# Kernel tuning notes

Hardware: AMD Instinct MI355X
Metric: run time of the kernel (lower is better)

Reference implementation:

```python
import jax, jax.numpy as jnp
import numpy as np

NUM_HEADS = 8
GROUPS = 32  # min(32, 512 // 4)
EPS = 1e-5


def group_norm(y, gamma, beta):
    B, C, L = y.shape
    yg = y.reshape(B, GROUPS, -1)  # [B, G, (C//G)*L]
    mu = yg.mean(-1, keepdims=True)
    var = yg.var(-1, keepdims=True)
    yn = ((yg - mu) * jax.lax.rsqrt(var + EPS)).reshape(B, C, L)
    return yn * gamma[:, None] + beta[:, None]


def setup_inputs() -> dict:
    key = jax.random.key(0)
    ks = jax.random.split(key, 5)
    B, C, L = 4, 512, 2048
    return {
        "x": jax.random.normal(ks[0], (B, C, L), dtype=jnp.float32),
        "Wqkv": jax.random.normal(ks[1], (3 * C, C), dtype=jnp.float32) * (C ** -0.5),
        "bqkv": jax.random.normal(ks[2], (3 * C,), dtype=jnp.float32) * 0.01,
        "Wproj": jax.random.normal(ks[3], (C, C), dtype=jnp.float32) * (C ** -0.5),
        "bproj": jax.random.normal(ks[4], (C,), dtype=jnp.float32) * 0.01,
        "gamma": jnp.ones((C,), dtype=jnp.float32),
        "beta": jnp.zeros((C,), dtype=jnp.float32),
    }


def reference(x, Wqkv, bqkv, Wproj, bproj, gamma, beta):
    B, C, L = x.shape
    H = NUM_HEADS
    D = C // H
    # 1x1 Conv1d == channel-mixing matmul
    qkv = jnp.einsum('oc,bcl->bol', Wqkv, x) + bqkv[:, None]  # [B, 3C, L]
    qkv = qkv.reshape(B, 3, H, D, L)
    q, k, v = qkv[:, 0], qkv[:, 1], qkv[:, 2]
    q = jnp.clip(q, -10.0, 10.0)
    k = jnp.clip(k, -10.0, 10.0)
    v = jnp.clip(v, -10.0, 10.0)
    scale = D ** -0.5
    attn = jnp.einsum('bhdi,bhdj->bhij', q, k) * scale  # [B, H, L, L]
    attn = jnp.clip(attn, -10.0, 10.0)
    attn = jax.nn.softmax(attn, axis=-1)
    # NaN fallback: replace whole attn with identity if any NaN (matches torch branch)
    has_nan = jnp.isnan(attn).any()
    attn = jnp.where(has_nan, jnp.eye(L, dtype=x.dtype), attn)
    out = jnp.einsum('bhij,bhdj->bhdi', attn, v)  # [B, H, D, L]
    out = out.reshape(B, C, L)
    out = jnp.einsum('oc,bcl->bol', Wproj, out) + bproj[:, None]
    return group_norm(out + x, gamma, beta)
```

## Files before the change

### kernel.cpp

```cpp
#include <hip/hip_runtime.h>
#include <cstddef>

#define B_ 4
#define C_ 512
#define L_ 2048

typedef __attribute__((ext_vector_type(8))) short  short8;
typedef __attribute__((ext_vector_type(4))) float  f32x4;
typedef __attribute__((ext_vector_type(4))) unsigned short us4;

#define AS1 __attribute__((address_space(1)))
#define AS3 __attribute__((address_space(3)))

__device__ __forceinline__ float clip10(float v){ return fminf(fmaxf(v,-10.0f),10.0f); }

__device__ __forceinline__ unsigned short f2bf(float f){
  union { float f; unsigned u; } v; v.f = f;
  unsigned r = v.u + 0x7fffu + ((v.u >> 16) & 1u);
  return (unsigned short)(r >> 16);
}
__device__ __forceinline__ unsigned pk(float lo, float hi){
  return (unsigned)f2bf(lo) | ((unsigned)f2bf(hi) << 16);
}
__device__ __forceinline__ void gl16(const void* g, void* l){
  __builtin_amdgcn_global_load_lds((const AS1 unsigned*)g, (AS3 unsigned*)l, 16, 0, 0);
}

__global__ __launch_bounds__(256) void prep_k(
    const float* __restrict__ x, const float* __restrict__ Wq,
    const float* __restrict__ Wp, unsigned short* __restrict__ xT,
    unsigned short* __restrict__ Wqb, unsigned short* __restrict__ Wpb)
{
  const int blk = blockIdx.x;
  const int t = threadIdx.x;
  if (blk < 4096){
    __shared__ float tile[32][33];
    const int b = blk>>10, rem = blk&1023;
    const int c0 = (rem>>6)*32, l0 = (rem&63)*32;
    const int cr = t>>3, lc = (t&7)*4;
    const float4 v = *(const float4*)(x + ((size_t)b*C_ + c0+cr)*L_ + l0 + lc);
    tile[cr][lc]=v.x; tile[cr][lc+1]=v.y; tile[cr][lc+2]=v.z; tile[cr][lc+3]=v.w;
    __syncthreads();
    const int lr = t>>3, cc = (t&7)*4;
    const us4 o = { f2bf(tile[cc][lr]), f2bf(tile[cc+1][lr]),
                    f2bf(tile[cc+2][lr]), f2bf(tile[cc+3][lr]) };
    *(us4*)(xT + ((size_t)b*L_ + l0+lr)*C_ + c0 + cc) = o;
  } else {
    const int i = (blk-4096)*256 + t;
    const int NQ = 1536*512/4;
    const float* src; unsigned short* dst; int j;
    if (i < NQ){ src = Wq; dst = Wqb; j = i; }
    else       { src = Wp; dst = Wpb; j = i - NQ; }
    const float4 v = *(const float4*)(src + (size_t)j*4);
    const us4 o = { f2bf(v.x), f2bf(v.y), f2bf(v.z), f2bf(v.w) };
    *(us4*)(dst + (size_t)j*4) = o;
  }
}

template<int MODE>
__global__ __launch_bounds__(256) void mfma_gemm(
    const unsigned short* __restrict__ Wb, const unsigned short* __restrict__ Bin,
    const float* __restrict__ bias,
    unsigned short* __restrict__ qT, unsigned short* __restrict__ kT,
    unsigned short* __restrict__ vN, float* __restrict__ yout)
{
  __shared__ unsigned short SA[128*64];
  __shared__ unsigned short SB[128*64];
  const int t = threadIdx.x;
  const int b = blockIdx.z;
  const int mb = blockIdx.y, n0 = blockIdx.x*128, m0 = mb*128;
  const int lane = t&63, w = t>>6, wm = w>>1, wn = w&1;
  const int n = lane&15, q4 = lane>>4;

  f32x4 acc[4][4];
#pragma unroll
  for (int i=0;i<4;i++)
#pragma unroll
    for (int j=0;j<4;j++) acc[i][j] = (f32x4){0.f,0.f,0.f,0.f};

  const unsigned short* Arow = Wb + (size_t)m0*512;
  const unsigned short* Brow = Bin + ((size_t)b*L_ + n0)*512;

  for (int kt=0; kt<8; kt++){
    const int k0 = kt*64;
    __syncthreads();
#pragma unroll
    for (int i=0;i<4;i++){
      const int ch = t + 256*i;
      const int row = ch>>3, lc = (ch&7) ^ (row&7);
      gl16(Arow + (size_t)row*512 + k0 + lc*8, &SA[ch*8]);
      gl16(Brow + (size_t)row*512 + k0 + lc*8, &SB[ch*8]);
    }
    __syncthreads();
#pragma unroll
    for (int kk=0;kk<2;kk++){
      short8 aF[4], bF[4];
      const int pc = ((kk*4+q4) ^ (n&7))*8;
#pragma unroll
      for (int mt=0;mt<4;mt++) aF[mt] = *(const short8*)&SA[(wm*64+mt*16+n)*64 + pc];
#pragma unroll
      for (int nt=0;nt<4;nt++) bF[nt] = *(const short8*)&SB[(wn*64+nt*16+n)*64 + pc];
#pragma unroll
      for (int mt=0;mt<4;mt++)
#pragma unroll
        for (int nt=0;nt<4;nt++)
          acc[mt][nt] = __builtin_amdgcn_mfma_f32_16x16x32_bf16(aF[mt], bF[nt], acc[mt][nt], 0,0,0);
    }
  }

#pragma unroll
  for (int mt=0;mt<4;mt++){
    const int obase = m0 + wm*64 + mt*16 + q4*4;
    const float b0=bias[obase], b1=bias[obase+1], b2=bias[obase+2], b3=bias[obase+3];
#pragma unroll
    for (int nt=0;nt<4;nt++){
      const int l = n0 + wn*64 + nt*16 + n;
      float r0=acc[mt][nt][0]+b0, r1=acc[mt][nt][1]+b1,
            r2=acc[mt][nt][2]+b2, r3=acc[mt][nt][3]+b3;
      if (MODE==0){
        r0=clip10(r0); r1=clip10(r1); r2=clip10(r2); r3=clip10(r3);
        const int typ = mb>>2;
        const int oin = obase - typ*512;
        if (typ < 2){
          unsigned short* dst = (typ==0) ? qT : kT;
          const us4 o = { f2bf(r0), f2bf(r1), f2bf(r2), f2bf(r3) };
          *(us4*)&dst[((size_t)b*L_ + l)*512 + oin] = o;
        } else {
          unsigned short* dst = vN + ((size_t)b*512 + oin)*L_ + l;
          dst[0]=f2bf(r0); dst[(size_t)L_]=f2bf(r1);
          dst[(size_t)2*L_]=f2bf(r2); dst[(size_t)3*L_]=f2bf(r3);
        }
      } else {
        float* dst = yout + ((size_t)b*512 + obase)*L_ + l;
        dst[0]=r0; dst[(size_t)L_]=r1; dst[(size_t)2*L_]=r2; dst[(size_t)3*L_]=r3;
      }
    }
  }
}

#define PP 72

__global__ __launch_bounds__(256) void attn_v4(
    const unsigned short* __restrict__ qT, const unsigned short* __restrict__ kT,
    const unsigned short* __restrict__ vN, unsigned short* __restrict__ attnT)
{
  __shared__ unsigned short s_p[128*PP];
  __shared__ unsigned short s_kv[2][2][64*64];
  const int t  = threadIdx.x;
  const int i0 = blockIdx.x*128;
  const int h  = blockIdx.y, b = blockIdx.z;
  const int lane = t&63, w = t>>6, n = lane&15, q4 = lane>>4;

  const unsigned short* kb0 = kT + (size_t)b*L_*512 + h*64;
  const unsigned short* vb  = vN + ((size_t)b*512 + h*64)*L_;

  short8 qf[2][2];
#pragma unroll
  for (int mt=0; mt<2; mt++)
#pragma unroll
    for (int kk=0; kk<2; kk++)
      qf[mt][kk] = *(const short8*)(qT + ((size_t)b*L_ + i0 + w*32 + mt*16 + n)*512
                                       + h*64 + kk*32 + q4*8);

#pragma unroll
  for (int i=0;i<2;i++){
    const int ch = t + 256*i, row = ch>>3, lc = (ch&7)^(row&7);
    gl16(kb0 + (size_t)row*512 + lc*8, &s_kv[0][0][ch*8]);
    gl16(vb  + (size_t)row*L_  + lc*8, &s_kv[0][1][ch*8]);
  }

  f32x4 oacc[2][4];
  float dacc[2];
#pragma unroll
  for (int mt=0;mt<2;mt++){ dacc[mt]=0.f;
#pragma unroll
    for (int dt=0;dt<4;dt++) oacc[mt][dt]=(f32x4){0.f,0.f,0.f,0.f}; }

  const float SCL = 0.125f*1.44269504089f;
  const float LIM = 14.4269504089f;

  int p = 0;
  for (int j0=0; j0<L_; j0+=64, p^=1){
    __syncthreads();
    if (j0+64 < L_){
#pragma unroll
      for (int i=0;i<2;i++){
        const int ch = t + 256*i, row = ch>>3, lc = (ch&7)^(row&7);
        gl16(kb0 + (size_t)(j0+64+row)*512 + lc*8,  &s_kv[p^1][0][ch*8]);
        gl16(vb  + (size_t)row*L_ + (j0+64) + lc*8, &s_kv[p^1][1][ch*8]);
      }
    }
    const unsigned short* sk = s_kv[p][0];
    const unsigned short* sv = s_kv[p][1];

    f32x4 sacc[2][4];
#pragma unroll
    for (int mt=0;mt<2;mt++)
#pragma unroll
      for (int jt=0;jt<4;jt++) sacc[mt][jt]=(f32x4){0.f,0.f,0.f,0.f};
#pragma unroll
    for (int kk=0;kk<2;kk++){
      const int pc = ((kk*4+q4) ^ (n&7))*8;
      short8 aK[4];
#pragma unroll
      for (int jt=0;jt<4;jt++) aK[jt] = *(const short8*)&sk[(jt*16+n)*64 + pc];
#pragma unroll
      for (int mt=0;mt<2;mt++)
#pragma unroll
        for (int jt=0;jt<4;jt++)
          sacc[mt][jt] = __builtin_amdgcn_mfma_f32_16x16x32_bf16(aK[jt], qf[mt][kk], sacc[mt][jt], 0,0,0);
    }

#pragma unroll
    for (int mt=0;mt<2;mt++)
#pragma unroll
      for (int jt=0;jt<4;jt++){
        const float e0 = __builtin_amdgcn_exp2f(__builtin_amdgcn_fmed3f(sacc[mt][jt][0]*SCL,-LIM,LIM));
        const float e1 = __builtin_amdgcn_exp2f(__builtin_amdgcn_fmed3f(sacc[mt][jt][1]*SCL,-LIM,LIM));
        const float e2 = __builtin_amdgcn_exp2f(__builtin_amdgcn_fmed3f(sacc[mt][jt][2]*SCL,-LIM,LIM));
        const float e3 = __builtin_amdgcn_exp2f(__builtin_amdgcn_fmed3f(sacc[mt][jt][3]*SCL,-LIM,LIM));
        dacc[mt] += (e0+e1)+(e2+e3);
        const unsigned long long pv =
            (unsigned long long)pk(e0,e1) | ((unsigned long long)pk(e2,e3)<<32);
        *(unsigned long long*)&s_p[(w*32 + mt*16 + n)*PP + jt*16 + q4*4] = pv;
      }

#pragma unroll
    for (int kk=0;kk<2;kk++){
      const int pcv = ((kk*4+q4) ^ (n&7))*8;
      short8 bV[4], pA[2];
#pragma unroll
      for (int dt=0;dt<4;dt++) bV[dt] = *(const short8*)&sv[(dt*16+n)*64 + pcv];
#pragma unroll
      for (int mt=0;mt<2;mt++)
        pA[mt] = *(const short8*)&s_p[(w*32 + mt*16 + n)*PP + kk*32 + q4*8];
#pragma unroll
      for (int mt=0;mt<2;mt++)
#pragma unroll
        for (int dt=0;dt<4;dt++)
          oacc[mt][dt] = __builtin_amdgcn_mfma_f32_16x16x32_bf16(pA[mt], bV[dt], oacc[mt][dt], 0,0,0);
    }
  }

  float inv[2];
#pragma unroll
  for (int mt=0;mt<2;mt++){
    float d = dacc[mt];
    d += __shfl_xor(d, 16);
    d += __shfl_xor(d, 32);
    inv[mt] = 1.0f/d;
  }
  float invr[2][4];
#pragma unroll
  for (int mt=0;mt<2;mt++)
#pragma unroll
    for (int r=0;r<4;r++)
      invr[mt][r] = __shfl(inv[mt], q4*4 + r);

#pragma unroll
  for (int mt=0;mt<2;mt++)
#pragma unroll
    for (int dt=0;dt<4;dt++)
#pragma unroll
      for (int r=0;r<4;r++){
        const size_t off = ((size_t)b*L_ + i0 + w*32 + mt*16 + q4*4 + r)*512 + h*64 + dt*16 + n;
        attnT[off] = f2bf(oacc[mt][dt][r]*invr[mt][r]);
      }
}

__global__ __launch_bounds__(256) void gn_stats(
    const float* __restrict__ y, const float* __restrict__ x,
    float* __restrict__ part)
{
  const int blk = blockIdx.x;
  const int b = blk>>7, g = (blk>>2)&31, s = blk&3;
  const size_t base = ((size_t)b*C_ + g*16)*L_ + s*512;
  const int t = threadIdx.x;
  float sum=0.f, sq=0.f;
#pragma unroll
  for (int i=0;i<8;i++){
    const int e = i*256 + t;
    const size_t off = base + (size_t)(e>>7)*L_ + (e&127)*4;
    const float4 vy=*(const float4*)(y+off);
    const float4 vx=*(const float4*)(x+off);
    const float a=vy.x+vx.x, c=vy.y+vx.y, d=vy.z+vx.z, f=vy.w+vx.w;
    sum += (a+c)+(d+f);
    sq  += (a*a+c*c)+(d*d+f*f);
  }
  for (int off=32;off>0;off>>=1){
    sum += __shfl_down(sum,off);
    sq  += __shfl_down(sq,off);
  }
  __shared__ float red[8];
  if ((t&63)==0){ red[(t>>6)*2]=sum; red[(t>>6)*2+1]=sq; }
  __syncthreads();
  if (t==0){
    part[blk*2+0] = red[0]+red[2]+red[4]+red[6];
    part[blk*2+1] = red[1]+red[3]+red[5]+red[7];
  }
}

__global__ __launch_bounds__(256) void gn_apply(
    const float* __restrict__ y, const float* __restrict__ x,
    const float* __restrict__ part,
    const float* __restrict__ gamma, const float* __restrict__ beta,
    float* __restrict__ out)
{
  const int blk = blockIdx.x;
  const int b = blk>>7, g = (blk>>2)&31, s = blk&3;
  const int bg8 = (blk & ~3)*2;
  const float sum = (part[bg8+0]+part[bg8+2])+(part[bg8+4]+part[bg8+6]);
  const float sq  = (part[bg8+1]+part[bg8+3])+(part[bg8+5]+part[bg8+7]);
  const float mu = sum*(1.0f/32768.0f);
  const float rs = rsqrtf(sq*(1.0f/32768.0f) - mu*mu + 1e-5f);
  const size_t base = ((size_t)b*C_ + g*16)*L_ + s*512;
  const int t = threadIdx.x;
#pragma unroll
  for (int i=0;i<8;i++){
    const int e = i*256 + t;
    const int row = e>>7;
    const size_t off = base + (size_t)row*L_ + (e&127)*4;
    const int c = g*16 + row;
    const float ga = gamma[c], be = beta[c];
    const float4 vy=*(const float4*)(y+off);
    const float4 vx=*(const float4*)(x+off);
    float4 r;
    r.x=((vy.x+vx.x)-mu)*rs*ga+be;
    r.y=((vy.y+vx.y)-mu)*rs*ga+be;
    r.z=((vy.z+vx.z)-mu)*rs*ga+be;
    r.w=((vy.w+vx.w)-mu)*rs*ga+be;
    *(float4*)(out+off)=r;
  }
}

extern "C" void kernel_launch(void* const* d_in, const int* in_sizes, int n_in,
                              void* d_out, int out_size, void* d_ws, size_t ws_size,
                              hipStream_t stream)
{
  (void)in_sizes; (void)n_in; (void)out_size; (void)ws_size;
  const float* x     = (const float*)d_in[0];
  const float* Wqkv  = (const float*)d_in[1];
  const float* bqkv  = (const float*)d_in[2];
  const float* Wproj = (const float*)d_in[3];
  const float* bproj = (const float*)d_in[4];
  const float* gamma = (const float*)d_in[5];
  const float* beta  = (const float*)d_in[6];
  float* out = (float*)d_out;
  char* ws = (char*)d_ws;

  const size_t MB = 1024*1024;
  unsigned short* qT    = (unsigned short*)(ws);
  unsigned short* kT    = (unsigned short*)(ws +  8*MB);
  unsigned short* vN    = (unsigned short*)(ws + 16*MB);
  unsigned short* attnT = (unsigned short*)(ws + 24*MB);
  unsigned short* xT    = (unsigned short*)(ws + 32*MB);
  unsigned short* Wqb   = (unsigned short*)(ws + 40*MB);
  unsigned short* Wpb   = (unsigned short*)(ws + 42*MB);
  float*          y     = (float*)        (ws + 43*MB);
  float*          part  = (float*)        (ws + 59*MB);

  prep_k      <<<dim3(5120),   256,0,stream>>>(x, Wqkv, Wproj, xT, Wqb, Wpb);
  mfma_gemm<0><<<dim3(16,12,4),256,0,stream>>>(Wqb, xT,    bqkv , qT,kT,vN, nullptr);
  attn_v4     <<<dim3(16,8,4), 256,0,stream>>>(qT, kT, vN, attnT);
  mfma_gemm<1><<<dim3(16, 4,4),256,0,stream>>>(Wpb, attnT, bproj, nullptr,nullptr,nullptr, y);
  gn_stats    <<<dim3(512),    256,0,stream>>>(y, x, part);
  gn_apply    <<<dim3(512),    256,0,stream>>>(y, x, part, gamma, beta, out);
}
```

Before: 201.3 us.

## Drop LDS staging: load MFMA operands directly from global memory

Both the GEMM and attention kernels stop staging K/V and weight tiles through LDS with async global-to-LDS copies and barriers. Instead each lane loads its MFMA fragments straight from global memory and relies on L1/L2 caching. The softmax scale is folded into Q at projection time, and bf16 packing of probabilities switches to truncation via a byte-permute. This removes barriers and LDS traffic but adds redundant global loads per wave, loses the explicit double-buffer prefetch, and truncation slightly changes numerics.

```diff
diff --git a/kernel.cpp b/kernel.cpp
--- a/kernel.cpp
+++ b/kernel.cpp
@@ -8,9 +8,6 @@
 typedef __attribute__((ext_vector_type(8))) short  short8;
 typedef __attribute__((ext_vector_type(4))) float  f32x4;
 typedef __attribute__((ext_vector_type(4))) unsigned short us4;
-
-#define AS1 __attribute__((address_space(1)))
-#define AS3 __attribute__((address_space(3)))
 
 __device__ __forceinline__ float clip10(float v){ return fminf(fmaxf(v,-10.0f),10.0f); }
 
@@ -19,11 +16,8 @@
   unsigned r = v.u + 0x7fffu + ((v.u >> 16) & 1u);
   return (unsigned short)(r >> 16);
 }
-__device__ __forceinline__ unsigned pk(float lo, float hi){
-  return (unsigned)f2bf(lo) | ((unsigned)f2bf(hi) << 16);
-}
-__device__ __forceinline__ void gl16(const void* g, void* l){
-  __builtin_amdgcn_global_load_lds((const AS1 unsigned*)g, (AS3 unsigned*)l, 16, 0, 0);
+__device__ __forceinline__ unsigned pk_tr(float lo, float hi){
+  return __builtin_amdgcn_perm(__float_as_uint(hi), __float_as_uint(lo), 0x07060302u);
 }
 
 __global__ __launch_bounds__(256) void prep_k(
@@ -64,8 +58,6 @@
     unsigned short* __restrict__ qT, unsigned short* __restrict__ kT,
     unsigned short* __restrict__ vN, float* __restrict__ yout)
 {
-  __shared__ unsigned short SA[128*64];
-  __shared__ unsigned short SB[128*64];
   const int t = threadIdx.x;
   const int b = blockIdx.z;
   const int mb = blockIdx.y, n0 = blockIdx.x*128, m0 = mb*128;
@@ -78,36 +70,30 @@
 #pragma unroll
     for (int j=0;j<4;j++) acc[i][j] = (f32x4){0.f,0.f,0.f,0.f};
 
-  const unsigned short* Arow = Wb + (size_t)m0*512;
-  const unsigned short* Brow = Bin + ((size_t)b*L_ + n0)*512;
-
-  for (int kt=0; kt<8; kt++){
-    const int k0 = kt*64;
-    __syncthreads();
-#pragma unroll
-    for (int i=0;i<4;i++){
-      const int ch = t + 256*i;
-      const int row = ch>>3, lc = (ch&7) ^ (row&7);
-      gl16(Arow + (size_t)row*512 + k0 + lc*8, &SA[ch*8]);
-      gl16(Brow + (size_t)row*512 + k0 + lc*8, &SB[ch*8]);
-    }
-    __syncthreads();
-#pragma unroll
-    for (int kk=0;kk<2;kk++){
-      short8 aF[4], bF[4];
-      const int pc = ((kk*4+q4) ^ (n&7))*8;
-#pragma unroll
-      for (int mt=0;mt<4;mt++) aF[mt] = *(const short8*)&SA[(wm*64+mt*16+n)*64 + pc];
-#pragma unroll
-      for (int nt=0;nt<4;nt++) bF[nt] = *(const short8*)&SB[(wn*64+nt*16+n)*64 + pc];
-#pragma unroll
-      for (int mt=0;mt<4;mt++)
-#pragma unroll
-        for (int nt=0;nt<4;nt++)
-          acc[mt][nt] = __builtin_amdgcn_mfma_f32_16x16x32_bf16(aF[mt], bF[nt], acc[mt][nt], 0,0,0);
-    }
-  }
-
+  const unsigned short* Ap[4];
+  const unsigned short* Bp[4];
+#pragma unroll
+  for (int mt=0;mt<4;mt++)
+    Ap[mt] = Wb + (size_t)(m0 + wm*64 + mt*16 + n)*512 + q4*8;
+#pragma unroll
+  for (int nt=0;nt<4;nt++)
+    Bp[nt] = Bin + ((size_t)b*L_ + n0 + wn*64 + nt*16 + n)*512 + q4*8;
+
+#pragma unroll 4
+  for (int k0=0;k0<512;k0+=32){
+    short8 aF[4], bF[4];
+#pragma unroll
+    for (int mt=0;mt<4;mt++) aF[mt] = *(const short8*)(Ap[mt] + k0);
+#pragma unroll
+    for (int nt=0;nt<4;nt++) bF[nt] = *(const short8*)(Bp[nt] + k0);
+#pragma unroll
+    for (int mt=0;mt<4;mt++)
+#pragma unroll
+      for (int nt=0;nt<4;nt++)
+        acc[mt][nt] = __builtin_amdgcn_mfma_f32_16x16x32_bf16(aF[mt], bF[nt], acc[mt][nt], 0,0,0);
+  }
+
+  const float QS = 0.180336880f;
 #pragma unroll
   for (int mt=0;mt<4;mt++){
     const int obase = m0 + wm*64 + mt*16 + q4*4;
@@ -122,6 +108,7 @@
         const int typ = mb>>2;
         const int oin = obase - typ*512;
         if (typ < 2){
+          if (typ==0){ r0*=QS; r1*=QS; r2*=QS; r3*=QS; }
           unsigned short* dst = (typ==0) ? qT : kT;
           const us4 o = { f2bf(r0), f2bf(r1), f2bf(r2), f2bf(r3) };
           *(us4*)&dst[((size_t)b*L_ + l)*512 + oin] = o;
@@ -140,19 +127,18 @@
 
 #define PP 72
 
-__global__ __launch_bounds__(256) void attn_v4(
+__global__ __launch_bounds__(256) void attn_v5(
     const unsigned short* __restrict__ qT, const unsigned short* __restrict__ kT,
     const unsigned short* __restrict__ vN, unsigned short* __restrict__ attnT)
 {
   __shared__ unsigned short s_p[128*PP];
-  __shared__ unsigned short s_kv[2][2][64*64];
   const int t  = threadIdx.x;
   const int i0 = blockIdx.x*128;
   const int h  = blockIdx.y, b = blockIdx.z;
   const int lane = t&63, w = t>>6, n = lane&15, q4 = lane>>4;
 
-  const unsigned short* kb0 = kT + (size_t)b*L_*512 + h*64;
-  const unsigned short* vb  = vN + ((size_t)b*512 + h*64)*L_;
+  const unsigned short* kb0 = kT + (size_t)b*L_*512 + h*64 + q4*8;
+  const unsigned short* vb  = vN + ((size_t)b*512 + h*64)*L_ + q4*8;
 
   short8 qf[2][2];
 #pragma unroll
@@ -162,12 +148,12 @@
       qf[mt][kk] = *(const short8*)(qT + ((size_t)b*L_ + i0 + w*32 + mt*16 + n)*512
                                        + h*64 + kk*32 + q4*8);
 
-#pragma unroll
-  for (int i=0;i<2;i++){
-    const int ch = t + 256*i, row = ch>>3, lc = (ch&7)^(row&7);
-    gl16(kb0 + (size_t)row*512 + lc*8, &s_kv[0][0][ch*8]);
-    gl16(vb  + (size_t)row*L_  + lc*8, &s_kv[0][1][ch*8]);
-  }
+  const unsigned short* kp[4];
+  const unsigned short* vp[4];
+#pragma unroll
+  for (int jt=0;jt<4;jt++) kp[jt] = kb0 + (size_t)(jt*16 + n)*512;
+#pragma unroll
+  for (int dt=0;dt<4;dt++) vp[dt] = vb  + (size_t)(dt*16 + n)*L_;
 
   f32x4 oacc[2][4];
   float dacc[2];
@@ -176,22 +162,15 @@
 #pragma unroll
     for (int dt=0;dt<4;dt++) oacc[mt][dt]=(f32x4){0.f,0.f,0.f,0.f}; }
 
-  const float SCL = 0.125f*1.44269504089f;
   const float LIM = 14.4269504089f;
 
-  int p = 0;
-  for (int j0=0; j0<L_; j0+=64, p^=1){
-    __syncthreads();
-    if (j0+64 < L_){
-#pragma unroll
-      for (int i=0;i<2;i++){
-        const int ch = t + 256*i, row = ch>>3, lc = (ch&7)^(row&7);
-        gl16(kb0 + (size_t)(j0+64+row)*512 + lc*8,  &s_kv[p^1][0][ch*8]);
-        gl16(vb  + (size_t)row*L_ + (j0+64) + lc*8, &s_kv[p^1][1][ch*8]);
-      }
-    }
-    const unsigned short* sk = s_kv[p][0];
-    const unsigned short* sv = s_kv[p][1];
+  for (int j0=0; j0<L_; j0+=64){
+    short8 aK[2][4];
+#pragma unroll
+    for (int kk=0;kk<2;kk++)
+#pragma unroll
+      for (int jt=0;jt<4;jt++)
+        aK[kk][jt] = *(const short8*)(kp[jt] + (size_t)j0*512 + kk*32);
 
     f32x4 sacc[2][4];
 #pragma unroll
@@ -199,38 +178,37 @@
 #pragma unroll
       for (int jt=0;jt<4;jt++) sacc[mt][jt]=(f32x4){0.f,0.f,0.f,0.f};
 #pragma unroll
-    for (int kk=0;kk<2;kk++){
-      const int pc = ((kk*4+q4) ^ (n&7))*8;
-      short8 aK[4];
-#pragma unroll
-      for (int jt=0;jt<4;jt++) aK[jt] = *(const short8*)&sk[(jt*16+n)*64 + pc];
+    for (int kk=0;kk<2;kk++)
 #pragma unroll
       for (int mt=0;mt<2;mt++)
 #pragma unroll
         for (int jt=0;jt<4;jt++)
-          sacc[mt][jt] = __builtin_amdgcn_mfma_f32_16x16x32_bf16(aK[jt], qf[mt][kk], sacc[mt][jt], 0,0,0);
-    }
+          sacc[mt][jt] = __builtin_amdgcn_mfma_f32_16x16x32_bf16(aK[kk][jt], qf[mt][kk], sacc[mt][jt], 0,0,0);
+
+    short8 bV[2][4];
+#pragma unroll
+    for (int kk=0;kk<2;kk++)
+#pragma unroll
+      for (int dt=0;dt<4;dt++)
+        bV[kk][dt] = *(const short8*)(vp[dt] + j0 + kk*32);
 
 #pragma unroll
     for (int mt=0;mt<2;mt++)
 #pragma unroll
       for (int jt=0;jt<4;jt++){
-        const float e0 = __builtin_amdgcn_exp2f(__builtin_amdgcn_fmed3f(sacc[mt][jt][0]*SCL,-LIM,LIM));
-        const float e1 = __builtin_amdgcn_exp2f(__builtin_amdgcn_fmed3f(sacc[mt][jt][1]*SCL,-LIM,LIM));
-        const float e2 = __builtin_amdgcn_exp2f(__builtin_amdgcn_fmed3f(sacc[mt][jt][2]*SCL,-LIM,LIM));
-        const float e3 = __builtin_amdgcn_exp2f(__builtin_amdgcn_fmed3f(sacc[mt][jt][3]*SCL,-LIM,LIM));
+        const float e0 = __builtin_amdgcn_exp2f(__builtin_amdgcn_fmed3f(sacc[mt][jt][0],-LIM,LIM));
+        const float e1 = __builtin_amdgcn_exp2f(__builtin_amdgcn_fmed3f(sacc[mt][jt][1],-LIM,LIM));
+        const float e2 = __builtin_amdgcn_exp2f(__builtin_amdgcn_fmed3f(sacc[mt][jt][2],-LIM,LIM));
+        const float e3 = __builtin_amdgcn_exp2f(__builtin_amdgcn_fmed3f(sacc[mt][jt][3],-LIM,LIM));
         dacc[mt] += (e0+e1)+(e2+e3);
         const unsigned long long pv =
-            (unsigned long long)pk(e0,e1) | ((unsigned long long)pk(e2,e3)<<32);
+            (unsigned long long)pk_tr(e0,e1) | ((unsigned long long)pk_tr(e2,e3)<<32);
         *(unsigned long long*)&s_p[(w*32 + mt*16 + n)*PP + jt*16 + q4*4] = pv;
       }
 
 #pragma unroll
     for (int kk=0;kk<2;kk++){
-      const int pcv = ((kk*4+q4) ^ (n&7))*8;
-      short8 bV[4], pA[2];
-#pragma unroll
-      for (int dt=0;dt<4;dt++) bV[dt] = *(const short8*)&sv[(dt*16+n)*64 + pcv];
+      short8 pA[2];
 #pragma unroll
       for (int mt=0;mt<2;mt++)
         pA[mt] = *(const short8*)&s_p[(w*32 + mt*16 + n)*PP + kk*32 + q4*8];
@@ -238,7 +216,7 @@
       for (int mt=0;mt<2;mt++)
 #pragma unroll
         for (int dt=0;dt<4;dt++)
-          oacc[mt][dt] = __builtin_amdgcn_mfma_f32_16x16x32_bf16(pA[mt], bV[dt], oacc[mt][dt], 0,0,0);
+          oacc[mt][dt] = __builtin_amdgcn_mfma_f32_16x16x32_bf16(pA[mt], bV[kk][dt], oacc[mt][dt], 0,0,0);
     }
   }
 
@@ -361,7 +339,7 @@
 
   prep_k      <<<dim3(5120),   256,0,stream>>>(x, Wqkv, Wproj, xT, Wqb, Wpb);
   mfma_gemm<0><<<dim3(16,12,4),256,0,stream>>>(Wqb, xT,    bqkv , qT,kT,vN, nullptr);
-  attn_v4     <<<dim3(16,8,4), 256,0,stream>>>(qT, kT, vN, attnT);
+  attn_v5     <<<dim3(16,8,4), 256,0,stream>>>(qT, kT, vN, attnT);
   mfma_gemm<1><<<dim3(16, 4,4),256,0,stream>>>(Wpb, attnT, bproj, nullptr,nullptr,nullptr, y);
   gn_stats    <<<dim3(512),    256,0,stream>>>(y, x, part);
   gn_apply    <<<dim3(512),    256,0,stream>>>(y, x, part, gamma, beta, out);
```

Result: slower. 297.7 us (+47.9%).

## Split attention key range across two blocks and combine partial sums

Applied to the files above, without the earlier changes.

Attention now splits the key dimension in two halves, one per block, doubling the grid to 1024 blocks. Each block writes unnormalized bf16 partial outputs and row denominators, and a new combine kernel sums and normalizes them. The softmax scale and log2e are folded into Q in the QKV GEMM epilogue, and bf16 packing switches to a truncating byte-permute instead of round-to-nearest. Double-buffered K/V loads are replaced by single buffers with two barriers per tile, trading prefetch overlap for higher occupancy (launch_bounds 256,4) at the cost of an extra kernel, extra global traffic, and some precision loss.

```diff
diff --git a/kernel.cpp b/kernel.cpp
--- a/kernel.cpp
+++ b/kernel.cpp
@@ -19,8 +19,11 @@
   unsigned r = v.u + 0x7fffu + ((v.u >> 16) & 1u);
   return (unsigned short)(r >> 16);
 }
-__device__ __forceinline__ unsigned pk(float lo, float hi){
-  return (unsigned)f2bf(lo) | ((unsigned)f2bf(hi) << 16);
+__device__ __forceinline__ unsigned pk_tr(float lo, float hi){
+  return __builtin_amdgcn_perm(__float_as_uint(hi), __float_as_uint(lo), 0x07060302u);
+}
+__device__ __forceinline__ float bf2f(unsigned short u){
+  return __uint_as_float(((unsigned)u)<<16);
 }
 __device__ __forceinline__ void gl16(const void* g, void* l){
   __builtin_amdgcn_global_load_lds((const AS1 unsigned*)g, (AS3 unsigned*)l, 16, 0, 0);
@@ -108,6 +111,7 @@
     }
   }
 
+  const float QS = 0.180336880f;
 #pragma unroll
   for (int mt=0;mt<4;mt++){
     const int obase = m0 + wm*64 + mt*16 + q4*4;
@@ -122,6 +126,7 @@
         const int typ = mb>>2;
         const int oin = obase - typ*512;
         if (typ < 2){
+          if (typ==0){ r0*=QS; r1*=QS; r2*=QS; r3*=QS; }
           unsigned short* dst = (typ==0) ? qT : kT;
           const us4 o = { f2bf(r0), f2bf(r1), f2bf(r2), f2bf(r3) };
           *(us4*)&dst[((size_t)b*L_ + l)*512 + oin] = o;
@@ -140,16 +145,20 @@
 
 #define PP 72
 
-__global__ __launch_bounds__(256) void attn_v4(
+__global__ __launch_bounds__(256,4) void attn_v8(
     const unsigned short* __restrict__ qT, const unsigned short* __restrict__ kT,
-    const unsigned short* __restrict__ vN, unsigned short* __restrict__ attnT)
-{
+    const unsigned short* __restrict__ vN,
+    unsigned short* __restrict__ Opart, float* __restrict__ den)
+{
+  __shared__ unsigned short s_k[64*64];
+  __shared__ unsigned short s_v[64*64];
   __shared__ unsigned short s_p[128*PP];
-  __shared__ unsigned short s_kv[2][2][64*64];
   const int t  = threadIdx.x;
-  const int i0 = blockIdx.x*128;
+  const int io = blockIdx.x>>1, half = blockIdx.x&1;
+  const int i0 = io*128;
   const int h  = blockIdx.y, b = blockIdx.z;
   const int lane = t&63, w = t>>6, n = lane&15, q4 = lane>>4;
+  const int idx = ((b*8+h)*16+io)*2 + half;
 
   const unsigned short* kb0 = kT + (size_t)b*L_*512 + h*64;
   const unsigned short* vb  = vN + ((size_t)b*512 + h*64)*L_;
@@ -162,13 +171,6 @@
       qf[mt][kk] = *(const short8*)(qT + ((size_t)b*L_ + i0 + w*32 + mt*16 + n)*512
                                        + h*64 + kk*32 + q4*8);
 
-#pragma unroll
-  for (int i=0;i<2;i++){
-    const int ch = t + 256*i, row = ch>>3, lc = (ch&7)^(row&7);
-    gl16(kb0 + (size_t)row*512 + lc*8, &s_kv[0][0][ch*8]);
-    gl16(vb  + (size_t)row*L_  + lc*8, &s_kv[0][1][ch*8]);
-  }
-
   f32x4 oacc[2][4];
   float dacc[2];
 #pragma unroll
@@ -176,22 +178,18 @@
 #pragma unroll
     for (int dt=0;dt<4;dt++) oacc[mt][dt]=(f32x4){0.f,0.f,0.f,0.f}; }
 
-  const float SCL = 0.125f*1.44269504089f;
   const float LIM = 14.4269504089f;
-
-  int p = 0;
-  for (int j0=0; j0<L_; j0+=64, p^=1){
-    __syncthreads();
-    if (j0+64 < L_){
-#pragma unroll
-      for (int i=0;i<2;i++){
-        const int ch = t + 256*i, row = ch>>3, lc = (ch&7)^(row&7);
-        gl16(kb0 + (size_t)(j0+64+row)*512 + lc*8,  &s_kv[p^1][0][ch*8]);
-        gl16(vb  + (size_t)row*L_ + (j0+64) + lc*8, &s_kv[p^1][1][ch*8]);
-      }
-    }
-    const unsigned short* sk = s_kv[p][0];
-    const unsigned short* sv = s_kv[p][1];
+  const int jbeg = half*1024, jend = jbeg+1024;
+
+  for (int j0=jbeg; j0<jend; j0+=64){
+    __syncthreads();
+#pragma unroll
+    for (int i=0;i<2;i++){
+      const int ch = t + 256*i, row = ch>>3, lc = (ch&7)^(row&7);
+      gl16(kb0 + (size_t)(j0+row)*512 + lc*8, &s_k[ch*8]);
+      gl16(vb  + (size_t)row*L_ + j0 + lc*8,  &s_v[ch*8]);
+    }
+    __syncthreads();
 
     f32x4 sacc[2][4];
 #pragma unroll
@@ -203,7 +201,7 @@
       const int pc = ((kk*4+q4) ^ (n&7))*8;
       short8 aK[4];
 #pragma unroll
-      for (int jt=0;jt<4;jt++) aK[jt] = *(const short8*)&sk[(jt*16+n)*64 + pc];
+      for (int jt=0;jt<4;jt++) aK[jt] = *(const short8*)&s_k[(jt*16+n)*64 + pc];
 #pragma unroll
       for (int mt=0;mt<2;mt++)
 #pragma unroll
@@ -215,13 +213,13 @@
     for (int mt=0;mt<2;mt++)
 #pragma unroll
       for (int jt=0;jt<4;jt++){
-        const float e0 = __builtin_amdgcn_exp2f(__builtin_amdgcn_fmed3f(sacc[mt][jt][0]*SCL,-LIM,LIM));
-        const float e1 = __builtin_amdgcn_exp2f(__builtin_amdgcn_fmed3f(sacc[mt][jt][1]*SCL,-LIM,LIM));
-        const float e2 = __builtin_amdgcn_exp2f(__builtin_amdgcn_fmed3f(sacc[mt][jt][2]*SCL,-LIM,LIM));
-        const float e3 = __builtin_amdgcn_exp2f(__builtin_amdgcn_fmed3f(sacc[mt][jt][3]*SCL,-LIM,LIM));
+        const float e0 = __builtin_amdgcn_exp2f(__builtin_amdgcn_fmed3f(sacc[mt][jt][0],-LIM,LIM));
+        const float e1 = __builtin_amdgcn_exp2f(__builtin_amdgcn_fmed3f(sacc[mt][jt][1],-LIM,LIM));
+        const float e2 = __builtin_amdgcn_exp2f(__builtin_amdgcn_fmed3f(sacc[mt][jt][2],-LIM,LIM));
+        const float e3 = __builtin_amdgcn_exp2f(__builtin_amdgcn_fmed3f(sacc[mt][jt][3],-LIM,LIM));
         dacc[mt] += (e0+e1)+(e2+e3);
         const unsigned long long pv =
-            (unsigned long long)pk(e0,e1) | ((unsigned long long)pk(e2,e3)<<32);
+            (unsigned long long)pk_tr(e0,e1) | ((unsigned long long)pk_tr(e2,e3)<<32);
         *(unsigned long long*)&s_p[(w*32 + mt*16 + n)*PP + jt*16 + q4*4] = pv;
       }
 
@@ -230,7 +228,7 @@
       const int pcv = ((kk*4+q4) ^ (n&7))*8;
       short8 bV[4], pA[2];
 #pragma unroll
-      for (int dt=0;dt<4;dt++) bV[dt] = *(const short8*)&sv[(dt*16+n)*64 + pcv];
+      for (int dt=0;dt<4;dt++) bV[dt] = *(const short8*)&s_v[(dt*16+n)*64 + pcv];
 #pragma unroll
       for (int mt=0;mt<2;mt++)
         pA[mt] = *(const short8*)&s_p[(w*32 + mt*16 + n)*PP + kk*32 + q4*8];
@@ -238,34 +236,54 @@
       for (int mt=0;mt<2;mt++)
 #pragma unroll
         for (int dt=0;dt<4;dt++)
-          oacc[mt][dt] = __builtin_amdgcn_mfma_f32_16x16x32_bf16(pA[mt], bV[dt], oacc[mt][dt], 0,0,0);
-    }
-  }
-
-  float inv[2];
+          oacc[mt][dt] = __builtin_amdgcn_mfma_f32_16x16x32_bf16(pA[mt], bV[kk==0?dt:dt], oacc[mt][dt], 0,0,0);
+    }
+  }
+
 #pragma unroll
   for (int mt=0;mt<2;mt++){
     float d = dacc[mt];
     d += __shfl_xor(d, 16);
     d += __shfl_xor(d, 32);
-    inv[mt] = 1.0f/d;
-  }
-  float invr[2][4];
+    if (q4 == 0) den[(size_t)idx*128 + w*32 + mt*16 + n] = d;
+  }
+
 #pragma unroll
   for (int mt=0;mt<2;mt++)
 #pragma unroll
-    for (int r=0;r<4;r++)
-      invr[mt][r] = __shfl(inv[mt], q4*4 + r);
-
-#pragma unroll
-  for (int mt=0;mt<2;mt++)
-#pragma unroll
     for (int dt=0;dt<4;dt++)
 #pragma unroll
-      for (int r=0;r<4;r++){
-        const size_t off = ((size_t)b*L_ + i0 + w*32 + mt*16 + q4*4 + r)*512 + h*64 + dt*16 + n;
-        attnT[off] = f2bf(oacc[mt][dt][r]*invr[mt][r]);
-      }
+      for (int r=0;r<4;r++)
+        Opart[(size_t)idx*8192 + (w*32 + mt*16 + q4*4 + r)*64 + dt*16 + n]
+            = f2bf(oacc[mt][dt][r]);
+}
+
+__global__ __launch_bounds__(256) void attn_combine(
+    const unsigned short* __restrict__ Opart, const float* __restrict__ den,
+    unsigned short* __restrict__ attnT)
+{
+  __shared__ float s_inv[128];
+  const int io = blockIdx.x, h = blockIdx.y, b = blockIdx.z;
+  const int t = threadIdx.x;
+  const int base = ((b*8+h)*16+io)*2;
+  if (t < 128)
+    s_inv[t] = 1.0f/(den[(size_t)base*128 + t] + den[(size_t)(base+1)*128 + t]);
+  __syncthreads();
+  const unsigned short* O0 = Opart + (size_t)base*8192;
+  const unsigned short* O1 = O0 + 8192;
+#pragma unroll
+  for (int it=0; it<8; it++){
+    const int chunk = it*256 + t;
+    const int i = chunk>>4, c4 = (chunk&15)*4;
+    const us4 a = *(const us4*)&O0[i*64 + c4];
+    const us4 c = *(const us4*)&O1[i*64 + c4];
+    const float inv = s_inv[i];
+    const us4 o = { f2bf((bf2f(a[0])+bf2f(c[0]))*inv),
+                    f2bf((bf2f(a[1])+bf2f(c[1]))*inv),
+                    f2bf((bf2f(a[2])+bf2f(c[2]))*inv),
+                    f2bf((bf2f(a[3])+bf2f(c[3]))*inv) };
+    *(us4*)&attnT[((size_t)b*L_ + io*128 + i)*512 + h*64 + c4] = o;
+  }
 }
 
 __global__ __launch_bounds__(256) void gn_stats(
@@ -354,14 +372,18 @@
   unsigned short* vN    = (unsigned short*)(ws + 16*MB);
   unsigned short* attnT = (unsigned short*)(ws + 24*MB);
   unsigned short* xT    = (unsigned short*)(ws + 32*MB);
+  float*          den   = (float*)        (ws + 32*MB);
   unsigned short* Wqb   = (unsigned short*)(ws + 40*MB);
   unsigned short* Wpb   = (unsigned short*)(ws + 42*MB);
   float*          y     = (float*)        (ws + 43*MB);
+  unsigned short* Opart = (unsigned short*)(ws + 43*MB);
   float*          part  = (float*)        (ws + 59*MB);
+
 
   prep_k      <<<dim3(5120),   256,0,stream>>>(x, Wqkv, Wproj, xT, Wqb, Wpb);
   mfma_gemm<0><<<dim3(16,12,4),256,0,stream>>>(Wqb, xT,    bqkv , qT,kT,vN, nullptr);
-  attn_v4     <<<dim3(16,8,4), 256,0,stream>>>(qT, kT, vN, attnT);
+  attn_v8     <<<dim3(32,8,4), 256,0,stream>>>(qT, kT, vN, Opart, den);
+  attn_combine<<<dim3(16,8,4), 256,0,stream>>>(Opart, den, attnT);
   mfma_gemm<1><<<dim3(16, 4,4),256,0,stream>>>(Wpb, attnT, bproj, nullptr,nullptr,nullptr, y);
   gn_stats    <<<dim3(512),    256,0,stream>>>(y, x, part);
   gn_apply    <<<dim3(512),    256,0,stream>>>(y, x, part, gamma, beta, out);
```

New measurement: 190.5 us. 5.4% less time.
